# Kernel optimization log

Hardware: AMD Instinct MI355X
Metric: run time of the kernel (lower is better)

The kernel has to match this reference:

```python
import jax, jax.numpy as jnp
import numpy as np

PRE_NMS_LIMIT = 6000
PROPOSAL_COUNT = 2000
NMS_THRESHOLD = 0.7
BBOX_STD = np.array([0.1, 0.1, 0.2, 0.2], dtype=np.float32)  # RPN_BBOX_STD_DEV


def setup_inputs() -> dict:
    key = jax.random.key(0)
    k1, k2, k3, k4 = jax.random.split(key, 4)
    B, N = 2, 262144
    # rpn_probs: softmax over (bg, fg) so column 1 is a valid fg probability
    rpn_probs = jax.nn.softmax(jax.random.normal(k1, (B, N, 2), dtype=jnp.float32), axis=-1)
    rpn_bbox = jax.random.normal(k2, (B, N, 4), dtype=jnp.float32)
    # anchors in normalized coords with y1<y2, x1<x2
    yx = jax.random.uniform(k3, (B, N, 2), dtype=jnp.float32) * 0.9
    hw = jax.random.uniform(k4, (B, N, 2), dtype=jnp.float32) * 0.1 + 0.005
    anchors = jnp.concatenate([yx, yx + hw], axis=-1)
    return {"rpn_probs": rpn_probs, "rpn_bbox": rpn_bbox, "anchors": anchors}


def _nms_single(boxes, scores):
    """Greedy NMS on score-sorted boxes [K,4]; returns [PROPOSAL_COUNT,4] padded."""
    K = boxes.shape[0]
    y1, x1, y2, x2 = boxes[:, 0], boxes[:, 1], boxes[:, 2], boxes[:, 3]
    areas = (y2 - y1) * (x2 - x1)
    iy1 = jnp.maximum(y1[:, None], y1[None, :])
    ix1 = jnp.maximum(x1[:, None], x1[None, :])
    iy2 = jnp.minimum(y2[:, None], y2[None, :])
    ix2 = jnp.minimum(x2[:, None], x2[None, :])
    inter = jnp.maximum(iy2 - iy1, 0.0) * jnp.maximum(ix2 - ix1, 0.0)
    union = areas[:, None] + areas[None, :] - inter
    iou = jnp.where(union > 0.0, inter / union, 0.0)  # [K, K]
    idxs = jnp.arange(K)

    def body(suppressed, xs):
        row, i = xs
        keep_i = jnp.logical_not(suppressed[i])
        suppressed = suppressed | (keep_i & (row > NMS_THRESHOLD) & (idxs > i))
        return suppressed, keep_i

    _, keep = jax.lax.scan(body, jnp.zeros((K,), bool), (iou, idxs))
    # gather kept boxes in score order, truncate/pad to PROPOSAL_COUNT
    rank = jnp.cumsum(keep) - 1
    valid = keep & (rank < PROPOSAL_COUNT)
    dest = jnp.where(valid, rank, PROPOSAL_COUNT)  # overflow bucket at index P
    out = jnp.zeros((PROPOSAL_COUNT + 1, 4), boxes.dtype)
    out = out.at[dest].set(jnp.where(valid[:, None], boxes, 0.0))
    return out[:PROPOSAL_COUNT]


def reference(rpn_probs, rpn_bbox, anchors):
    scores = rpn_probs[:, :, 1]  # fg prob [B, N]
    deltas = rpn_bbox * jnp.asarray(BBOX_STD).reshape(1, 1, 4)
    k = min(PRE_NMS_LIMIT, anchors.shape[1])
    top_scores, ix = jax.lax.top_k(scores, k)  # sorted desc, [B, K]
    gather = lambda a: jnp.take_along_axis(a, ix[..., None], axis=1)
    d = gather(deltas)       # [B, K, 4]
    a = gather(anchors)      # [B, K, 4]
    # apply_box_deltas_graph (vectorized over batch)
    h = a[..., 2] - a[..., 0]
    w = a[..., 3] - a[..., 1]
    cy = a[..., 0] + 0.5 * h + d[..., 0] * h
    cx = a[..., 1] + 0.5 * w + d[..., 1] * w
    h = h * jnp.exp(d[..., 2])
    w = w * jnp.exp(d[..., 3])
    y1 = cy - 0.5 * h
    x1 = cx - 0.5 * w
    boxes = jnp.stack([y1, x1, y1 + h, x1 + w], axis=-1)
    # clip to window (0, 0, 1, 1)
    boxes = jnp.clip(boxes, 0.0, 1.0)
    proposals = jax.vmap(_nms_single)(boxes, top_scores)  # [B, P, 4]
    return proposals
```

## Files before the change

### kernel.cpp

```cpp
#include <hip/hip_runtime.h>
#include <stdint.h>

typedef unsigned long long u64;

#define NB 2
#define N_ANCHORS 262144
#define LOG2N 18
#define PRE_NMS 6000
#define PROPOSALS 2000
#define NCHUNK 94
#define CAND_CAP 8192
#define HBINS 16384
#define HB_BLOCKS_PER_B 64
#define HB_CHUNK (N_ANCHORS / HB_BLOCKS_PER_B)
#define CB_BLOCKS_PER_B 64
#define CB_CHUNK (N_ANCHORS / CB_BLOCKS_PER_B)
#define CBUF 512
#define EDGE_CAP 65536
#define EDGE_LDS 16384

#define OFF_HIST 0
#define OFF_BCNT (NB*HBINS*4)
#define OFF_SCAL (2*NB*HBINS*4)
#define ZERO_BYTES (OFF_SCAL + 256)
#define OFF_CAND ZERO_BYTES
#define OFF_SUFF (OFF_CAND + NB*CAND_CAP*8)
#define OFF_BOXES (OFF_SUFF + NB*HBINS*4)
#define OFF_EDGES (OFF_BOXES + NB*PRE_NMS*16)


__global__ __launch_bounds__(256) void zero_ws(uint4* __restrict__ p) {
    int i = blockIdx.x * 256 + threadIdx.x;
    if (i < ZERO_BYTES / 16) p[i] = make_uint4(0u, 0u, 0u, 0u);
}

__global__ __launch_bounds__(256) void hist_kernel(const float4* __restrict__ probs4,
                                                   unsigned* __restrict__ hist) {
    __shared__ unsigned lh[HBINS];
    int t = threadIdx.x;
    for (int j = t; j < HBINS; j += 256) lh[j] = 0u;
    __syncthreads();
    int b   = blockIdx.x / HB_BLOCKS_PER_B;
    int blk = blockIdx.x % HB_BLOCKS_PER_B;
    const float4* p = probs4 + ((size_t)b * N_ANCHORS + (size_t)blk * HB_CHUNK) / 2;
    #pragma unroll 4
    for (int k = 0; k < HB_CHUNK / 512; ++k) {
        float4 v = p[k * 256 + t];
        unsigned bin0 = __float_as_uint(v.y) >> 16;
        unsigned bin1 = __float_as_uint(v.w) >> 16;
        if (bin0 > HBINS - 1) bin0 = HBINS - 1;
        if (bin1 > HBINS - 1) bin1 = HBINS - 1;
        atomicAdd(&lh[bin0], 1u);
        atomicAdd(&lh[bin1], 1u);
    }
    __syncthreads();
    unsigned* gh = hist + (size_t)b * HBINS;
    for (int j = t; j < HBINS; j += 256) {
        unsigned v = lh[j];
        if (v) atomicAdd(&gh[j], v);
    }
}

__global__ __launch_bounds__(1024) void scan_sel(const unsigned* __restrict__ hist,
                                                 int* __restrict__ scal,
                                                 unsigned* __restrict__ suff) {
    int b = blockIdx.x;
    const unsigned* h = hist + (size_t)b * HBINS;
    unsigned* sf = suff + (size_t)b * HBINS;
    int t = threadIdx.x;
    unsigned base = t * 16;
    unsigned hl[16];
    unsigned s = 0;
    #pragma unroll
    for (int j = 0; j < 16; ++j) { hl[j] = h[base + j]; s += hl[j]; }
    __shared__ unsigned buf[1024];
    buf[t] = s;
    __syncthreads();
    for (int off = 1; off < 1024; off <<= 1) {
        unsigned v = buf[t] + ((t + off < 1024) ? buf[t + off] : 0u);
        __syncthreads();
        buf[t] = v;
        __syncthreads();
    }
    unsigned run = (t < 1023) ? buf[t + 1] : 0u;
    #pragma unroll
    for (int j = 15; j >= 0; --j) {
        sf[base + j] = run;
        run += hl[j];
    }
    unsigned sufInc = buf[t];
    unsigned sufBefore = sufInc - s;
    if (sufBefore < PRE_NMS && sufInc >= PRE_NMS) {
        unsigned r2 = sufBefore;
        unsigned T = 0, totC = 0;
        for (int j = 15; j >= 0; --j) {
            if (r2 + hl[j] >= PRE_NMS) { T = base + j; totC = r2 + hl[j]; break; }
            r2 += hl[j];
        }
        if (totC > CAND_CAP) totC = CAND_CAP;
        scal[b * 8 + 2] = (int)(T << 16);
        scal[b * 8 + 6] = (int)totC;
    }
}

__global__ __launch_bounds__(256) void compact(const float4* __restrict__ probs4,
                                               const int* __restrict__ scal,
                                               const unsigned* __restrict__ suff,
                                               unsigned* __restrict__ binCnt,
                                               u64* __restrict__ cand) {
    __shared__ unsigned lcnt[HBINS];
    __shared__ u64 keyBuf[CBUF];
    __shared__ unsigned slotBuf[CBUF];
    __shared__ int nc;
    int t = threadIdx.x;
    int b   = blockIdx.x / CB_BLOCKS_PER_B;
    int blk = blockIdx.x % CB_BLOCKS_PER_B;
    for (int j = t; j < HBINS; j += 256) lcnt[j] = 0u;
    if (t == 0) nc = 0;
    __syncthreads();
    unsigned kthr = (unsigned)scal[b * 8 + 2];
    const unsigned* sfB = suff + (size_t)b * HBINS;
    unsigned* bcB = binCnt + (size_t)b * HBINS;
    u64* candB = cand + (size_t)b * CAND_CAP;
    size_t anchor0 = (size_t)blk * CB_CHUNK;
    const float4* p = probs4 + ((size_t)b * N_ANCHORS + anchor0) / 2;
    #pragma unroll 2
    for (int k = 0; k < CB_CHUNK / 512; ++k) {
        float4 v = p[k * 256 + t];
        unsigned n0 = (unsigned)(anchor0 + ((size_t)(k * 256 + t)) * 2);
        unsigned keys[2] = { __float_as_uint(v.y), __float_as_uint(v.w) };
        #pragma unroll
        for (int e = 0; e < 2; ++e) {
            unsigned key = keys[e];
            if (key >= kthr) {
                unsigned bin = key >> 16;
                u64 k64 = ((u64)key << 32) | (u64)(~(n0 + e));
                int idx = atomicAdd(&nc, 1);
                if (idx < CBUF) {
                    unsigned slot = atomicAdd(&lcnt[bin], 1u);
                    keyBuf[idx] = k64;
                    slotBuf[idx] = slot;
                } else {
                    unsigned gs = atomicAdd(&bcB[bin], 1u);
                    unsigned pos = sfB[bin] + gs;
                    if (pos < CAND_CAP) candB[pos] = k64;
                }
            }
        }
    }
    __syncthreads();
    for (int j = t; j < HBINS; j += 256) {
        unsigned c = lcnt[j];
        if (c) lcnt[j] = atomicAdd(&bcB[j], c);
    }
    __syncthreads();
    int tot = nc < CBUF ? nc : CBUF;
    for (int k = t; k < tot; k += 256) {
        u64 k64 = keyBuf[k];
        unsigned bin = (unsigned)(k64 >> 48);
        unsigned pos = sfB[bin] + lcnt[bin] + slotBuf[k];
        if (pos < CAND_CAP) candB[pos] = k64;
    }
}

__global__ __launch_bounds__(256) void refine_decode(const u64* __restrict__ cand,
                                                     const int* __restrict__ scal,
                                                     const unsigned* __restrict__ suff,
                                                     const unsigned* __restrict__ binCnt,
                                                     const float* __restrict__ anchors,
                                                     const float* __restrict__ bbox,
                                                     float4* __restrict__ boxes) {
    int b = blockIdx.y;
    int wave = threadIdx.x >> 6;
    int lane = threadIdx.x & 63;
    int p = blockIdx.x * 4 + wave;
    if (p >= scal[b * 8 + 6]) return;
    u64 my = cand[(size_t)b * CAND_CAP + p];
    unsigned bin = (unsigned)(my >> 48);
    unsigned s = suff[(size_t)b * HBINS + bin];
    if (s >= PRE_NMS) return;
    unsigned c = binCnt[(size_t)b * HBINS + bin];
    if (s + c > CAND_CAP) c = CAND_CAP - s;
    const u64* seg = cand + (size_t)b * CAND_CAP + s;
    int cnt = 0;
    for (unsigned q = lane; q < c; q += 64)
        cnt += (seg[q] > my) ? 1 : 0;
    #pragma unroll
    for (int off = 32; off; off >>= 1) cnt += __shfl_down(cnt, off, 64);
    int rank = (int)s + __shfl(cnt, 0, 64);
    if (rank < PRE_NMS && lane == 0) {
        int n = (int)(~(unsigned)(my & 0xFFFFFFFFull));
        const float4* anch4 = (const float4*)anchors + (size_t)b * N_ANCHORS;
        const float4* bb4   = (const float4*)bbox    + (size_t)b * N_ANCHORS;
        float4 a  = anch4[n];
        float4 dd = bb4[n];
        float d0 = dd.x * 0.1f, d1 = dd.y * 0.1f;
        float d2 = dd.z * 0.2f, d3 = dd.w * 0.2f;
        float h = a.z - a.x, w = a.w - a.y;
        float cy = a.x + 0.5f * h + d0 * h;
        float cx = a.y + 0.5f * w + d1 * w;
        h = h * expf(d2);
        w = w * expf(d3);
        float y1 = cy - 0.5f * h, x1 = cx - 0.5f * w;
        float y2 = y1 + h,        x2 = x1 + w;
        y1 = fminf(fmaxf(y1, 0.f), 1.f);
        x1 = fminf(fmaxf(x1, 0.f), 1.f);
        y2 = fminf(fmaxf(y2, 0.f), 1.f);
        x2 = fminf(fmaxf(x2, 0.f), 1.f);
        boxes[(size_t)b * PRE_NMS + rank] = make_float4(y1, x1, y2, x2);
    }
}

__global__ __launch_bounds__(256) void iou_edges(const float4* __restrict__ boxes,
                                                 int* __restrict__ scal,
                                                 unsigned* __restrict__ edges) {
    int c  = blockIdx.x;
    int rb = blockIdx.y;
    int b  = blockIdx.z;
    int rowBase = rb * 256;
    if (rowBase >= (c + 1) * 64) return;
    const float4* bx = boxes + (size_t)b * PRE_NMS;
    __shared__ float4 cb[64];
    __shared__ float  ca[64];
    int t = threadIdx.x;
    if (t < 64) {
        int col = c * 64 + t;
        float4 v = (col < PRE_NMS) ? bx[col] : make_float4(2.f, 2.f, 2.f, 2.f);
        cb[t] = v;
        ca[t] = (v.z - v.x) * (v.w - v.y);
    }
    __syncthreads();
    int i = rowBase + t;
    if (i >= PRE_NMS) return;
    int rel = i - c * 64;
    u64 maskGT = (rel < 0) ? ~0ull : ((rel >= 63) ? 0ull : ~((2ull << rel) - 1ull));
    if (!maskGT) return;
    float4 bi = bx[i];
    float ai = (bi.z - bi.x) * (bi.w - bi.y);
    u64 m = 0ull;
    #pragma unroll
    for (int j = 0; j < 64; ++j) {
        float4 bj = cb[j];
        float iy1 = fmaxf(bi.x, bj.x);
        float ix1 = fmaxf(bi.y, bj.y);
        float iy2 = fminf(bi.z, bj.z);
        float ix2 = fminf(bi.w, bj.w);
        float inter = fmaxf(iy2 - iy1, 0.f) * fmaxf(ix2 - ix1, 0.f);
        float uni = ai + ca[j] - inter;
        if (inter > 0.7f * uni) m |= (1ull << j);
    }
    m &= maskGT;
    while (m) {
        int j = __ffsll((long long)m) - 1;
        m &= m - 1;
        int col = c * 64 + j;
        int pos = atomicAdd(&scal[b * 8 + 5], 1);
        if (pos < EDGE_CAP)
            edges[(size_t)b * EDGE_CAP + pos] = ((unsigned)col << 16) | (unsigned)i;
    }
}

__global__ __launch_bounds__(256) void nms_fix(const unsigned* __restrict__ edges,
                                               const int* __restrict__ scal,
                                               const float4* __restrict__ boxes,
                                               float4* __restrict__ out) {
    int b = blockIdx.x;
    int t = threadIdx.x;
    int E = scal[b * 8 + 5];
    if (E > EDGE_CAP) E = EDGE_CAP;
    __shared__ u64 S[NCHUNK];
    __shared__ u64 Snew[NCHUNK];
    __shared__ unsigned eL[EDGE_LDS];
    __shared__ int changed;
    __shared__ int pref[NCHUNK];
    __shared__ int totalKept;
    const unsigned* eg = edges + (size_t)b * EDGE_CAP;
    bool staged = (E <= EDGE_LDS);
    if (staged) for (int k = t; k < E; k += 256) eL[k] = eg[k];
    for (int w = t; w < NCHUNK; w += 256) S[w] = 0ull;
    __syncthreads();
    if (E > 0) {
        for (int it = 0; it < PRE_NMS + 1; ++it) {
            for (int w = t; w < NCHUNK; w += 256) Snew[w] = 0ull;
            if (t == 0) changed = 0;
            __syncthreads();
            for (int k = t; k < E; k += 256) {
                unsigned e = staged ? eL[k] : eg[k];
                int i = (int)(e & 0xFFFFu), j = (int)(e >> 16);
                if (!((S[i >> 6] >> (i & 63)) & 1ull))
                    atomicOr(&Snew[j >> 6], 1ull << (j & 63));
            }
            __syncthreads();
            int ch = 0;
            for (int w = t; w < NCHUNK; w += 256) {
                if (Snew[w] != S[w]) { ch = 1; S[w] = Snew[w]; }
            }
            if (ch) changed = 1;
            __syncthreads();
            if (!changed) break;
        }
    }
    for (int w = t; w < NCHUNK; w += 256) {
        u64 valid = (w < NCHUNK - 1) ? ~0ull : ((1ull << (PRE_NMS - (NCHUNK - 1) * 64)) - 1ull);
        Snew[w] = (~S[w]) & valid;
    }
    __syncthreads();
    if (t == 0) {
        int run = 0;
        for (int w = 0; w < NCHUNK; ++w) { pref[w] = run; run += __popcll(Snew[w]); }
        totalKept = (run < PROPOSALS) ? run : PROPOSALS;
    }
    __syncthreads();
    const float4* bx = boxes + (size_t)b * PRE_NMS;
    float4* ob = out + (size_t)b * PROPOSALS;
    if (t < NCHUNK) {
        u64 k = Snew[t];
        int pos = pref[t];
        while (k && pos < PROPOSALS) {
            int l = __ffsll((long long)k) - 1;
            k &= k - 1;
            ob[pos++] = bx[t * 64 + l];
        }
    }
    int tk = totalKept;
    for (int q = tk + t; q < PROPOSALS; q += 256)
        ob[q] = make_float4(0.f, 0.f, 0.f, 0.f);
}

extern "C" void kernel_launch(void* const* d_in, const int* in_sizes, int n_in,
                              void* d_out, int out_size, void* d_ws, size_t ws_size,
                              hipStream_t stream) {
    (void)in_sizes; (void)n_in; (void)out_size; (void)ws_size;
    const float4* probs4 = (const float4*)d_in[0];
    const float* bbox    = (const float*)d_in[1];
    const float* anchors = (const float*)d_in[2];
    char* ws = (char*)d_ws;
    unsigned* hist   = (unsigned*)(ws + OFF_HIST);
    unsigned* binCnt = (unsigned*)(ws + OFF_BCNT);
    int* scal        = (int*)(ws + OFF_SCAL);
    u64* cand        = (u64*)(ws + OFF_CAND);
    unsigned* suff   = (unsigned*)(ws + OFF_SUFF);
    float4* boxes    = (float4*)(ws + OFF_BOXES);
    unsigned* edges  = (unsigned*)(ws + OFF_EDGES);

    zero_ws<<<(ZERO_BYTES / 16 + 255) / 256, 256, 0, stream>>>((uint4*)ws);

    hist_kernel<<<NB * HB_BLOCKS_PER_B, 256, 0, stream>>>(probs4, hist);
    scan_sel<<<NB, 1024, 0, stream>>>(hist, scal, suff);
    compact<<<NB * CB_BLOCKS_PER_B, 256, 0, stream>>>(probs4, scal, suff, binCnt, cand);
    refine_decode<<<dim3(CAND_CAP / 4, NB), 256, 0, stream>>>(cand, scal, suff, binCnt,
                                                              anchors, bbox, boxes);
    dim3 gIou(NCHUNK, (PRE_NMS + 255) / 256, NB);
    iou_edges<<<gIou, 256, 0, stream>>>(boxes, scal, edges);
    nms_fix<<<NB, 256, 0, stream>>>(edges, scal, boxes, (float4*)d_out);
}
```

Measured before the change: 82.57 us.

## Replace global histogram atomics with per-block rows and a reduce pass

Each histogram block now writes its full local histogram to its own row, and a new reduce kernel sums the rows, instead of issuing global atomics. This removes the separate zeroing kernel: the bin counters and the scalar are cleared inside scan_sel. The compact kernel's LDS counter array shrinks to a 2048-bin window above the threshold bin, with out-of-window keys falling back to global atomics, which lowers LDS init and flush cost. The cost is extra global traffic of 2x64x16384 words written and then read back, plus one more launch.

After: 76.04 us. 7.9% less time.

```diff
diff --git a/kernel.cpp b/kernel.cpp
--- a/kernel.cpp
+++ b/kernel.cpp
@@ -16,26 +16,22 @@
 #define CB_BLOCKS_PER_B 64
 #define CB_CHUNK (N_ANCHORS / CB_BLOCKS_PER_B)
 #define CBUF 512
+#define WINDOW 2048
 #define EDGE_CAP 65536
 #define EDGE_LDS 16384
 
 #define OFF_HIST 0
 #define OFF_BCNT (NB*HBINS*4)
 #define OFF_SCAL (2*NB*HBINS*4)
-#define ZERO_BYTES (OFF_SCAL + 256)
-#define OFF_CAND ZERO_BYTES
+#define OFF_CAND (OFF_SCAL + 256)
 #define OFF_SUFF (OFF_CAND + NB*CAND_CAP*8)
 #define OFF_BOXES (OFF_SUFF + NB*HBINS*4)
 #define OFF_EDGES (OFF_BOXES + NB*PRE_NMS*16)
-
-
-__global__ __launch_bounds__(256) void zero_ws(uint4* __restrict__ p) {
-    int i = blockIdx.x * 256 + threadIdx.x;
-    if (i < ZERO_BYTES / 16) p[i] = make_uint4(0u, 0u, 0u, 0u);
-}
+#define OFF_HROWS (OFF_EDGES + NB*EDGE_CAP*4)
+
 
 __global__ __launch_bounds__(256) void hist_kernel(const float4* __restrict__ probs4,
-                                                   unsigned* __restrict__ hist) {
+                                                   unsigned* __restrict__ hrows) {
     __shared__ unsigned lh[HBINS];
     int t = threadIdx.x;
     for (int j = t; j < HBINS; j += 256) lh[j] = 0u;
@@ -54,20 +50,33 @@
         atomicAdd(&lh[bin1], 1u);
     }
     __syncthreads();
-    unsigned* gh = hist + (size_t)b * HBINS;
-    for (int j = t; j < HBINS; j += 256) {
-        unsigned v = lh[j];
-        if (v) atomicAdd(&gh[j], v);
-    }
+    unsigned* row = hrows + (size_t)(b * HB_BLOCKS_PER_B + blk) * HBINS;
+    for (int j = t; j < HBINS; j += 256) row[j] = lh[j];
+}
+
+__global__ __launch_bounds__(256) void hist_reduce(const unsigned* __restrict__ hrows,
+                                                   unsigned* __restrict__ hist) {
+    int b   = blockIdx.x / (HBINS / 256);
+    int blk = blockIdx.x % (HBINS / 256);
+    int bin = blk * 256 + threadIdx.x;
+    const unsigned* base = hrows + (size_t)b * HB_BLOCKS_PER_B * HBINS + bin;
+    unsigned s = 0;
+    #pragma unroll 8
+    for (int r = 0; r < HB_BLOCKS_PER_B; ++r) s += base[(size_t)r * HBINS];
+    hist[(size_t)b * HBINS + bin] = s;
 }
 
 __global__ __launch_bounds__(1024) void scan_sel(const unsigned* __restrict__ hist,
                                                  int* __restrict__ scal,
-                                                 unsigned* __restrict__ suff) {
+                                                 unsigned* __restrict__ suff,
+                                                 unsigned* __restrict__ binCnt) {
     int b = blockIdx.x;
     const unsigned* h = hist + (size_t)b * HBINS;
     unsigned* sf = suff + (size_t)b * HBINS;
-    int t = threadIdx.x;
+    unsigned* bc = binCnt + (size_t)b * HBINS;
+    int t = threadIdx.x;
+    for (int j = t; j < HBINS; j += 1024) bc[j] = 0u;
+    if (t == 0) scal[b * 8 + 5] = 0;
     unsigned base = t * 16;
     unsigned hl[16];
     unsigned s = 0;
@@ -108,17 +117,18 @@
                                                const unsigned* __restrict__ suff,
                                                unsigned* __restrict__ binCnt,
                                                u64* __restrict__ cand) {
-    __shared__ unsigned lcnt[HBINS];
+    __shared__ unsigned lcnt[WINDOW];
     __shared__ u64 keyBuf[CBUF];
     __shared__ unsigned slotBuf[CBUF];
     __shared__ int nc;
     int t = threadIdx.x;
     int b   = blockIdx.x / CB_BLOCKS_PER_B;
     int blk = blockIdx.x % CB_BLOCKS_PER_B;
-    for (int j = t; j < HBINS; j += 256) lcnt[j] = 0u;
+    for (int j = t; j < WINDOW; j += 256) lcnt[j] = 0u;
     if (t == 0) nc = 0;
     __syncthreads();
     unsigned kthr = (unsigned)scal[b * 8 + 2];
+    unsigned T = kthr >> 16;
     const unsigned* sfB = suff + (size_t)b * HBINS;
     unsigned* bcB = binCnt + (size_t)b * HBINS;
     u64* candB = cand + (size_t)b * CAND_CAP;
@@ -134,10 +144,11 @@
             unsigned key = keys[e];
             if (key >= kthr) {
                 unsigned bin = key >> 16;
+                unsigned rel = bin - T;
                 u64 k64 = ((u64)key << 32) | (u64)(~(n0 + e));
-                int idx = atomicAdd(&nc, 1);
-                if (idx < CBUF) {
-                    unsigned slot = atomicAdd(&lcnt[bin], 1u);
+                int idx;
+                if (rel < WINDOW && (idx = atomicAdd(&nc, 1)) < CBUF) {
+                    unsigned slot = atomicAdd(&lcnt[rel], 1u);
                     keyBuf[idx] = k64;
                     slotBuf[idx] = slot;
                 } else {
@@ -149,16 +160,16 @@
         }
     }
     __syncthreads();
-    for (int j = t; j < HBINS; j += 256) {
+    for (int j = t; j < WINDOW; j += 256) {
         unsigned c = lcnt[j];
-        if (c) lcnt[j] = atomicAdd(&bcB[j], c);
+        if (c) lcnt[j] = atomicAdd(&bcB[T + j], c);
     }
     __syncthreads();
     int tot = nc < CBUF ? nc : CBUF;
     for (int k = t; k < tot; k += 256) {
         u64 k64 = keyBuf[k];
         unsigned bin = (unsigned)(k64 >> 48);
-        unsigned pos = sfB[bin] + lcnt[bin] + slotBuf[k];
+        unsigned pos = sfB[bin] + lcnt[bin - T] + slotBuf[k];
         if (pos < CAND_CAP) candB[pos] = k64;
     }
 }
@@ -342,11 +353,11 @@
     unsigned* suff   = (unsigned*)(ws + OFF_SUFF);
     float4* boxes    = (float4*)(ws + OFF_BOXES);
     unsigned* edges  = (unsigned*)(ws + OFF_EDGES);
-
-    zero_ws<<<(ZERO_BYTES / 16 + 255) / 256, 256, 0, stream>>>((uint4*)ws);
-
-    hist_kernel<<<NB * HB_BLOCKS_PER_B, 256, 0, stream>>>(probs4, hist);
-    scan_sel<<<NB, 1024, 0, stream>>>(hist, scal, suff);
+    unsigned* hrows  = (unsigned*)(ws + OFF_HROWS);
+
+    hist_kernel<<<NB * HB_BLOCKS_PER_B, 256, 0, stream>>>(probs4, hrows);
+    hist_reduce<<<NB * (HBINS / 256), 256, 0, stream>>>(hrows, hist);
+    scan_sel<<<NB, 1024, 0, stream>>>(hist, scal, suff, binCnt);
     compact<<<NB * CB_BLOCKS_PER_B, 256, 0, stream>>>(probs4, scal, suff, binCnt, cand);
     refine_decode<<<dim3(CAND_CAP / 4, NB), 256, 0, stream>>>(cand, scal, suff, binCnt,
                                                               anchors, bbox, boxes);
```
